# Kernel tuning notes

Hardware: AMD Instinct MI355X
Metric: run time of the kernel (lower is better)

Reference implementation:

```python
import jax, jax.numpy as jnp
import numpy as np

NEG_SLOPE = 0.2
BN_EPS = 1e-5


def gat_conv(x, W_src, W_dst, att_src, att_dst, bias, src, dst, num_nodes):
    # PyG GATConv, heads=1, concat=True, self-loops already included in (src,dst)
    h_src = x @ W_src                      # [N, H]
    h_dst = x @ W_dst                      # [N, H]
    a_src = h_src @ att_src                # [N]
    a_dst = h_dst @ att_dst                # [N]
    e = jax.nn.leaky_relu(a_src[src] + a_dst[dst], NEG_SLOPE)   # [E]
    # segment softmax over incoming edges of each dst node
    m = jax.ops.segment_max(e, dst, num_segments=num_nodes)     # [N]
    p = jnp.exp(e - m[dst])
    denom = jax.ops.segment_sum(p, dst, num_segments=num_nodes) # [N]
    alpha = p / denom[dst]                                      # [E]
    msgs = alpha[:, None] * h_src[src]                           # [E, H]
    out = jax.ops.segment_sum(msgs, dst, num_segments=num_nodes)
    return out + bias


def setup_inputs() -> dict:
    key = jax.random.key(0)
    ks = jax.random.split(key, 20)
    N, D_IN, H1, H2, FC, C = 100000, 256, 128, 128, 64, 40
    E = 1600000
    inp = {}
    inp['x'] = jax.random.normal(ks[0], (N, D_IN), dtype=jnp.float32)
    inp['edge_index'] = jax.random.randint(ks[1], (2, E), 0, N, dtype=jnp.int64)
    s = 1.0 / np.sqrt(D_IN)
    inp['W1_src'] = jax.random.uniform(ks[2], (D_IN, H1), jnp.float32, -s, s)
    inp['W1_dst'] = jax.random.uniform(ks[3], (D_IN, H1), jnp.float32, -s, s)
    inp['att1_src'] = jax.random.normal(ks[4], (H1,), jnp.float32) * 0.1
    inp['att1_dst'] = jax.random.normal(ks[5], (H1,), jnp.float32) * 0.1
    inp['b1'] = jnp.zeros((H1,), jnp.float32)
    s = 1.0 / np.sqrt(H1)
    inp['W2_src'] = jax.random.uniform(ks[6], (H1, H2), jnp.float32, -s, s)
    inp['W2_dst'] = jax.random.uniform(ks[7], (H1, H2), jnp.float32, -s, s)
    inp['att2_src'] = jax.random.normal(ks[8], (H2,), jnp.float32) * 0.1
    inp['att2_dst'] = jax.random.normal(ks[9], (H2,), jnp.float32) * 0.1
    inp['b2'] = jnp.zeros((H2,), jnp.float32)
    s = 1.0 / np.sqrt(H2)
    inp['fc1_w'] = jax.random.uniform(ks[10], (H2, FC), jnp.float32, -s, s)
    inp['fc1_b'] = jax.random.uniform(ks[11], (FC,), jnp.float32, -s, s)
    inp['gamma'] = jnp.ones((FC,), jnp.float32)
    inp['beta'] = jnp.zeros((FC,), jnp.float32)
    s = 1.0 / np.sqrt(FC)
    inp['fc2_w'] = jax.random.uniform(ks[12], (FC, C), jnp.float32, -s, s)
    inp['fc2_b'] = jax.random.uniform(ks[13], (C,), jnp.float32, -s, s)
    return inp


def reference(x, edge_index, W1_src, W1_dst, att1_src, att1_dst, b1,
              W2_src, W2_dst, att2_src, att2_dst, b2,
              fc1_w, fc1_b, gamma, beta, fc2_w, fc2_b):
    N = x.shape[0]
    loops = jnp.arange(N, dtype=edge_index.dtype)
    src = jnp.concatenate([edge_index[0], loops])
    dst = jnp.concatenate([edge_index[1], loops])
    h = jax.nn.relu(gat_conv(x, W1_src, W1_dst, att1_src, att1_dst, b1, src, dst, N))
    h = jax.nn.relu(gat_conv(h, W2_src, W2_dst, att2_src, att2_dst, b2, src, dst, N))
    h = h @ fc1_w + fc1_b                   # [N, 64]
    mu = jnp.mean(h, axis=0)
    var = jnp.var(h, axis=0)
    h = (h - mu) * jax.lax.rsqrt(var + BN_EPS) * gamma + beta
    h = jax.nn.relu(h)
    h = h @ fc2_w + fc2_b                   # [N, C]
    return jax.nn.log_softmax(h, axis=-1)
```

## Files before the change

### kernel.cpp

```cpp
#include <hip/hip_runtime.h>
#include <cstddef>

#define LSLOPE 0.2f
#define BN_EPS 1e-5f

__device__ __forceinline__ float lrelu(float x) { return x > 0.f ? x : LSLOPE * x; }

using half4 = __attribute__((ext_vector_type(4))) _Float16;
using half8 = __attribute__((ext_vector_type(8))) _Float16;
using f32x4 = __attribute__((ext_vector_type(4))) float;

struct h2 { _Float16 h, l; };
__device__ __forceinline__ h2 split2h(float x) {
  h2 r;
  r.h = (_Float16)x;
  r.l = (_Float16)(x - (float)r.h);
  return r;
}

__device__ __forceinline__ unsigned short f2bf(float x) {
  unsigned u = __float_as_uint(x);
  unsigned r = (u + 0x7fffu + ((u >> 16) & 1u)) >> 16;
  return (unsigned short)r;
}
__device__ __forceinline__ float bflo(unsigned int u) { return __uint_as_float(u << 16); }
__device__ __forceinline__ float bfhi(unsigned int u) { return __uint_as_float(u & 0xffff0000u); }

__device__ __forceinline__ void bfrag_body(const float* __restrict__ B, _Float16* __restrict__ bh,
                                           _Float16* __restrict__ bl, int K, int M, int t) {
  int KB = K >> 5;
  int CTF = M >> 4;
  int lane = t & 63;
  int ckb  = t >> 6;
  int c  = ckb / KB, kb = ckb % KB;
  int mr = lane & 15, quad = lane >> 4;
  int col = c * 16 + mr;
  size_t obase = ((size_t)kb * CTF + c) * 512 + (size_t)lane * 8;
#pragma unroll
  for (int j = 0; j < 8; ++j) {
    int k = kb * 32 + quad * 8 + j;
    h2 s = split2h(B[(size_t)k * M + col]);
    bh[obase + j] = s.h;
    bl[obase + j] = s.l;
  }
}

__device__ __forceinline__ void matvec_body(const float* __restrict__ A, const float* __restrict__ v,
                                            float* __restrict__ out, int R, int K, int t) {
  int w = t >> 6;
  int lane = t & 63;
  if (w >= R) return;
  const float* row = A + (size_t)w * K;
  float s = 0.f;
  for (int k = lane; k < K; k += 64) s = fmaf(row[k], v[k], s);
#pragma unroll
  for (int off = 32; off; off >>= 1) s += __shfl_xor(s, off, 64);
  if (lane == 0) out[w] = s;
}

__global__ __launch_bounds__(256) void prep_k(const float* __restrict__ W1s, const float* __restrict__ W2s,
                                              const float* __restrict__ fc1w,
                                              const float* __restrict__ W1d, const float* __restrict__ att1d,
                                              const float* __restrict__ W2d, const float* __restrict__ att2d,
                                              const float* __restrict__ att1s, const float* __restrict__ att2s,
                                              _Float16* B1h, _Float16* B1l, _Float16* B2h, _Float16* B2l,
                                              _Float16* Bfh, _Float16* Bfl,
                                              float* wvd1, float* wvd2, float* wvs1, float* wvs2) {
  int b = blockIdx.x;
  int tid = threadIdx.x;
  if (b < 16)       bfrag_body(W1s, B1h, B1l, 256, 128, b * 256 + tid);
  else if (b < 24)  bfrag_body(W2s, B2h, B2l, 128, 128, (b - 16) * 256 + tid);
  else if (b < 28)  bfrag_body(fc1w, Bfh, Bfl, 128, 64, (b - 24) * 256 + tid);
  else if (b < 92)  matvec_body(W1d, att1d, wvd1, 256, 128, (b - 28) * 256 + tid);
  else if (b < 124) matvec_body(W2d, att2d, wvd2, 128, 128, (b - 92) * 256 + tid);
  else if (b < 188) matvec_body(W1s, att1s, wvs1, 256, 128, (b - 124) * 256 + tid);
  else              matvec_body(W2s, att2s, wvs2, 128, 128, (b - 188) * 256 + tid);
}

template<int K, int MCOLS, bool PS>
__global__ __launch_bounds__(256) void gemm_sk(const float* __restrict__ Af,
                                               const _Float16* __restrict__ Ah,
                                               const _Float16* __restrict__ Al,
                                               const _Float16* __restrict__ Bh,
                                               const _Float16* __restrict__ Bl,
                                               float* __restrict__ Cf,
                                               unsigned short* __restrict__ Cbf,
                                               const float* __restrict__ wvs,
                                               float* __restrict__ asrc,
                                               const float* __restrict__ wvd,
                                               float* __restrict__ adout,
                                               int N,
                                               const float* __restrict__ bias) {
  constexpr int KB   = K / 32;
  constexpr int HALF = MCOLS / 2;
  constexpr int CT   = HALF / 16;
  constexpr int CTF  = MCOLS / 16;
  constexpr int BCH  = CTF / 4;
  __shared__ __align__(16) _Float16 sAh[2][64 * 32];
  __shared__ __align__(16) _Float16 sAl[2][64 * 32];
  __shared__ __align__(16) _Float16 sBh[2][CTF * 512];
  __shared__ __align__(16) _Float16 sBl[2][CTF * 512];
  const int tid  = threadIdx.x;
  const int row0 = blockIdx.x * 64;
  const int wv   = tid >> 6;
  const int wm   = wv >> 1;
  const int wn   = wv & 1;
  const int lane = tid & 63;
  const int quad = lane >> 4;
  const int mr   = lane & 15;

  f32x4 acc[2][CT];
#pragma unroll
  for (int r = 0; r < 2; ++r)
#pragma unroll
    for (int c = 0; c < CT; ++c) acc[r][c] = (f32x4){0.f, 0.f, 0.f, 0.f};
  float pas[2] = {0.f, 0.f}, pad[2] = {0.f, 0.f};

  auto stage_b = [&](int buf, int kbs) {
    const size_t gb = (size_t)kbs * (CTF * 512) + (size_t)lane * 8;
#pragma unroll
    for (int pch = 0; pch < BCH; ++pch) {
      const int ch = wv * BCH + pch;
      __builtin_amdgcn_global_load_lds(
          (const __attribute__((address_space(1))) void*)(Bh + gb + (size_t)ch * 512),
          (__attribute__((address_space(3))) void*)&sBh[buf][ch * 512], 16, 0, 0);
      __builtin_amdgcn_global_load_lds(
          (const __attribute__((address_space(1))) void*)(Bl + gb + (size_t)ch * 512),
          (__attribute__((address_space(3))) void*)&sBl[buf][ch * 512], 16, 0, 0);
    }
  };

  int srow, skc, soff;
  bool sok;
  if (PS) {
    srow = tid >> 2;
    skc  = (tid & 3) << 3;
  } else {
    srow = tid >> 3;
    skc  = (tid & 7) << 2;
  }
  soff = srow * 32 + ((skc + srow * 8) & 31);
  sok  = (row0 + srow) < N;
  int srow2 = 0, skc2 = 0, soff2 = 0;
  bool sok2 = false;
  if (!PS) {
    int s = tid + 256;
    srow2 = s >> 3;
    skc2  = (s & 7) << 2;
    soff2 = srow2 * 32 + ((skc2 + srow2 * 8) & 31);
    sok2  = (row0 + srow2) < N;
  }

  const float4 zf4 = make_float4(0.f, 0.f, 0.f, 0.f);
  const uint4  zu4 = make_uint4(0u, 0u, 0u, 0u);

  stage_b(0, 0);

  {
    if (PS) {
      size_t go = (size_t)(row0 + srow) * K + skc;
      uint4 h0 = sok ? *(const uint4*)&Ah[go] : zu4;
      uint4 l0 = sok ? *(const uint4*)&Al[go] : zu4;
      *(uint4*)&sAh[0][soff] = h0;
      *(uint4*)&sAl[0][soff] = l0;
    } else {
      float4 f0 = sok  ? *(const float4*)&Af[(size_t)(row0 + srow) * K + skc]   : zf4;
      float4 f1 = sok2 ? *(const float4*)&Af[(size_t)(row0 + srow2) * K + skc2] : zf4;
      h2 s0 = split2h(f0.x), s1 = split2h(f0.y), s2 = split2h(f0.z), s3 = split2h(f0.w);
      half4 h4, l4;
      h4[0] = s0.h; h4[1] = s1.h; h4[2] = s2.h; h4[3] = s3.h;
      l4[0] = s0.l; l4[1] = s1.l; l4[2] = s2.l; l4[3] = s3.l;
      *(half4*)&sAh[0][soff] = h4;
      *(half4*)&sAl[0][soff] = l4;
      h2 t0 = split2h(f1.x), t1 = split2h(f1.y), t2 = split2h(f1.z), t3 = split2h(f1.w);
      h4[0] = t0.h; h4[1] = t1.h; h4[2] = t2.h; h4[3] = t3.h;
      l4[0] = t0.l; l4[1] = t1.l; l4[2] = t2.l; l4[3] = t3.l;
      *(half4*)&sAh[0][soff2] = h4;
      *(half4*)&sAl[0][soff2] = l4;
    }
  }

  float4 fa0 = zf4, fa1 = zf4, fb0 = zf4, fb1 = zf4;
  uint4  uah = zu4, ual = zu4, ubh = zu4, ubl = zu4;
  if (KB > 1) {
    const int kn = 32;
    if (PS) {
      size_t go = (size_t)(row0 + srow) * K + kn + skc;
      uah = sok ? *(const uint4*)&Ah[go] : zu4;
      ual = sok ? *(const uint4*)&Al[go] : zu4;
    } else {
      fa0 = sok  ? *(const float4*)&Af[(size_t)(row0 + srow) * K + kn + skc]   : zf4;
      fa1 = sok2 ? *(const float4*)&Af[(size_t)(row0 + srow2) * K + kn + skc2] : zf4;
    }
  }
  __syncthreads();

  const size_t cstride = (size_t)KB * 512;

  for (int kb = 0; kb < KB; ++kb) {
    const int cur = kb & 1, nxt = cur ^ 1;
    const int kk = kb << 5;
    if (kb + 1 < KB) stage_b(nxt, kb + 1);
    if (kb + 2 < KB) {
      const int kn = (kb + 2) << 5;
      if (PS) {
        size_t go = (size_t)(row0 + srow) * K + kn + skc;
        ubh = sok ? *(const uint4*)&Ah[go] : zu4;
        ubl = sok ? *(const uint4*)&Al[go] : zu4;
      } else {
        fb0 = sok  ? *(const float4*)&Af[(size_t)(row0 + srow) * K + kn + skc]   : zf4;
        fb1 = sok2 ? *(const float4*)&Af[(size_t)(row0 + srow2) * K + kn + skc2] : zf4;
      }
    }

    half8 ah[2], al[2];
#pragma unroll
    for (int r = 0; r < 2; ++r) {
      int row = wm * 32 + r * 16 + mr;
      int off = row * 32 + ((quad + row) & 3) * 8;
      ah[r] = *(const half8*)&sAh[cur][off];
      al[r] = *(const half8*)&sAl[cur][off];
    }
    if (wn == 0 && (wvs || wvd)) {
#pragma unroll
      for (int j = 0; j < 8; ++j) {
        const float vs = wvs ? wvs[kk + quad * 8 + j] : 0.f;
        const float vd = wvd ? wvd[kk + quad * 8 + j] : 0.f;
#pragma unroll
        for (int r = 0; r < 2; ++r) {
          const float av = (float)ah[r][j] + (float)al[r][j];
          if (wvs) pas[r] = fmaf(av, vs, pas[r]);
          if (wvd) pad[r] = fmaf(av, vd, pad[r]);
        }
      }
    }
#pragma unroll
    for (int c = 0; c < CT; ++c) {
      const half8 bh = *(const half8*)&sBh[cur][(wn * CT + c) * 512 + lane * 8];
      const half8 bl = *(const half8*)&sBl[cur][(wn * CT + c) * 512 + lane * 8];
#pragma unroll
      for (int r = 0; r < 2; ++r) {
        f32x4 a = acc[r][c];
        a = __builtin_amdgcn_mfma_f32_16x16x32_f16(al[r], bh, a, 0, 0, 0);
        a = __builtin_amdgcn_mfma_f32_16x16x32_f16(ah[r], bl, a, 0, 0, 0);
        a = __builtin_amdgcn_mfma_f32_16x16x32_f16(ah[r], bh, a, 0, 0, 0);
        acc[r][c] = a;
      }
    }
    if (kb + 1 < KB) {
      if (PS) {
        *(uint4*)&sAh[nxt][soff] = uah;
        *(uint4*)&sAl[nxt][soff] = ual;
        uah = ubh; ual = ubl;
      } else {
        h2 s0 = split2h(fa0.x), s1 = split2h(fa0.y), s2 = split2h(fa0.z), s3 = split2h(fa0.w);
        half4 h4, l4;
        h4[0] = s0.h; h4[1] = s1.h; h4[2] = s2.h; h4[3] = s3.h;
        l4[0] = s0.l; l4[1] = s1.l; l4[2] = s2.l; l4[3] = s3.l;
        *(half4*)&sAh[nxt][soff] = h4;
        *(half4*)&sAl[nxt][soff] = l4;
        h2 t0 = split2h(fa1.x), t1 = split2h(fa1.y), t2 = split2h(fa1.z), t3 = split2h(fa1.w);
        h4[0] = t0.h; h4[1] = t1.h; h4[2] = t2.h; h4[3] = t3.h;
        l4[0] = t0.l; l4[1] = t1.l; l4[2] = t2.l; l4[3] = t3.l;
        *(half4*)&sAh[nxt][soff2] = h4;
        *(half4*)&sAl[nxt][soff2] = l4;
        fa0 = fb0; fa1 = fb1;
      }
    }
    __syncthreads();
  }

#pragma unroll
  for (int r = 0; r < 2; ++r)
#pragma unroll
    for (int c = 0; c < CT; ++c) {
      const int gcol = wn * HALF + c * 16 + mr;
      const float bv = bias ? bias[gcol] : 0.f;
#pragma unroll
      for (int q = 0; q < 4; ++q) {
        const int grow = row0 + wm * 32 + r * 16 + quad * 4 + q;
        if (grow < N) {
          float val = acc[r][c][q] + bv;
          if (Cf)  Cf[(size_t)grow * MCOLS + gcol] = val;
          if (Cbf) Cbf[(size_t)grow * 128 + gcol] = f2bf(val);
        }
      }
    }
  if (wn == 0 && wvs) {
#pragma unroll
    for (int r = 0; r < 2; ++r) {
      float d = pas[r];
      d += __shfl_xor(d, 16, 64);
      d += __shfl_xor(d, 32, 64);
      const int grow = row0 + wm * 32 + r * 16 + mr;
      if (quad == 0 && grow < N) asrc[grow] = d;
    }
  }
  if (wn == 0 && wvd) {
#pragma unroll
    for (int r = 0; r < 2; ++r) {
      float d = pad[r];
      d += __shfl_xor(d, 16, 64);
      d += __shfl_xor(d, 32, 64);
      const int grow = row0 + wm * 32 + r * 16 + mr;
      if (quad == 0 && grow < N) adout[grow] = d;
    }
  }
}

__global__ void deg_count_k(const int* __restrict__ edst, int E, int N, int* __restrict__ deg) {
  int i = blockIdx.x * 256 + threadIdx.x;
  if (i >= E + N) return;
  int d = (i < E) ? edst[i] : (i - E);
  atomicAdd(&deg[d], 1);
}

__global__ __launch_bounds__(1024) void scan1_k(const int* __restrict__ deg, int n,
                                                int* __restrict__ ex, int* __restrict__ bsum) {
  __shared__ int sm[1024];
  int t = threadIdx.x;
  int idx = blockIdx.x * 1024 + t;
  int v = (idx < n) ? deg[idx] : 0;
  sm[t] = v;
  __syncthreads();
  for (int off = 1; off < 1024; off <<= 1) {
    int tv = (t >= off) ? sm[t - off] : 0;
    __syncthreads();
    sm[t] += tv;
    __syncthreads();
  }
  if (idx < n) ex[idx] = sm[t] - v;
  if (t == 1023) bsum[blockIdx.x] = sm[t];
}

__global__ void scan3_k(int* __restrict__ ex, const int* __restrict__ bsum, int n, int nb, int total,
                        int* __restrict__ cursor) {
  __shared__ int pbase[2];
  int idx = blockIdx.x * 256 + threadIdx.x;
  int bin0 = (blockIdx.x * 256) >> 10;
  if (threadIdx.x < 2) {
    int b = bin0 + threadIdx.x;
    int s = 0;
    for (int i = 0; i < b && i < nb; ++i) s += bsum[i];
    pbase[threadIdx.x] = s;
  }
  __syncthreads();
  if (idx < n) {
    int v = ex[idx] + pbase[(idx >> 10) - bin0];
    ex[idx] = v;
    cursor[idx] = v;
  }
  if (idx == 0) ex[n] = total;
}

__global__ void scatter_range_k(const int* __restrict__ esrc, const int* __restrict__ edst,
                                int E, int N, int d0, int d1,
                                int* __restrict__ cursor, int* __restrict__ csr_src) {
  int i = blockIdx.x * 256 + threadIdx.x;
  if (i >= E + N) return;
  int d = (i < E) ? edst[i] : (i - E);
  if (d < d0 || d >= d1) return;
  int s = (i < E) ? esrc[i] : d;
  int pos = atomicAdd(&cursor[d], 1);
  csr_src[pos] = s;
}

__global__ __launch_bounds__(256) void gat_agg_k(const unsigned short* __restrict__ hbf,
                                                 const float* __restrict__ a_src,
                                                 const float* __restrict__ a_dst, const int* __restrict__ rowstart,
                                                 const int* __restrict__ csr_src, const float* __restrict__ bias,
                                                 _Float16* __restrict__ oh, _Float16* __restrict__ ol,
                                                 const float* __restrict__ wvd, float* __restrict__ ad_out,
                                                 int N) {
  int w = (blockIdx.x * blockDim.x + threadIdx.x) >> 6;
  int lane = threadIdx.x & 63;
  if (w >= N) return;
  int s0 = rowstart[w];
  int s1 = rowstart[w + 1];
  int deg = s1 - s0;
  float ad = a_dst[w];

  int sA = 0;
  float eA = -3.0e38f;
  if (lane < deg) {
    sA = csr_src[s0 + lane];
    eA = lrelu(a_src[sA] + ad);
  }
  float m = eA;
  for (int j = s0 + 64 + lane; j < s1; j += 64) {
    int s = csr_src[j];
    m = fmaxf(m, lrelu(a_src[s] + ad));
  }
#pragma unroll
  for (int off = 32; off; off >>= 1) m = fmaxf(m, __shfl_xor(m, off, 64));

  float preg = (lane < deg) ? __expf(eA - m) : 0.f;
  float den = preg;
  for (int j = s0 + 64 + lane; j < s1; j += 64) {
    int s = csr_src[j];
    den += __expf(lrelu(a_src[s] + ad) - m);
  }
#pragma unroll
  for (int off = 32; off; off >>= 1) den += __shfl_xor(den, off, 64);
  float inv = 1.f / den;

  const int q  = lane >> 4;
  const int sl = lane & 15;
  const uint4* hrow4 = (const uint4*)hbf;
  float acc[8];
#pragma unroll
  for (int i = 0; i < 8; ++i) acc[i] = 0.f;

  int lim  = deg < 64 ? deg : 64;
  int lim4 = (lim + 3) & ~3;
  int   sP = __shfl(sA, q, 64);
  float wP = __shfl(preg, q, 64) * inv;
  uint4 uP = hrow4[(size_t)sP * 16 + sl];
  for (int jj = 4; jj < lim4; jj += 4) {
    int   sN = __shfl(sA, jj + q, 64);
    float wN = __shfl(preg, jj + q, 64) * inv;
    uint4 uN = hrow4[(size_t)sN * 16 + sl];
    acc[0] = fmaf(wP, bflo(uP.x), acc[0]);
    acc[1] = fmaf(wP, bfhi(uP.x), acc[1]);
    acc[2] = fmaf(wP, bflo(uP.y), acc[2]);
    acc[3] = fmaf(wP, bfhi(uP.y), acc[3]);
    acc[4] = fmaf(wP, bflo(uP.z), acc[4]);
    acc[5] = fmaf(wP, bfhi(uP.z), acc[5]);
    acc[6] = fmaf(wP, bflo(uP.w), acc[6]);
    acc[7] = fmaf(wP, bfhi(uP.w), acc[7]);
    uP = uN; wP = wN;
  }
  acc[0] = fmaf(wP, bflo(uP.x), acc[0]);
  acc[1] = fmaf(wP, bfhi(uP.x), acc[1]);
  acc[2] = fmaf(wP, bflo(uP.y), acc[2]);
  acc[3] = fmaf(wP, bfhi(uP.y), acc[3]);
  acc[4] = fmaf(wP, bflo(uP.z), acc[4]);
  acc[5] = fmaf(wP, bfhi(uP.z), acc[5]);
  acc[6] = fmaf(wP, bflo(uP.w), acc[6]);
  acc[7] = fmaf(wP, bfhi(uP.w), acc[7]);

  for (int j = s0 + 64 + q; j < s1; j += 4) {
    int s = csr_src[j];
    float wgt = __expf(lrelu(a_src[s] + ad) - m) * inv;
    uint4 u = hrow4[(size_t)s * 16 + sl];
    acc[0] = fmaf(wgt, bflo(u.x), acc[0]);
    acc[1] = fmaf(wgt, bfhi(u.x), acc[1]);
    acc[2] = fmaf(wgt, bflo(u.y), acc[2]);
    acc[3] = fmaf(wgt, bfhi(u.y), acc[3]);
    acc[4] = fmaf(wgt, bflo(u.z), acc[4]);
    acc[5] = fmaf(wgt, bfhi(u.z), acc[5]);
    acc[6] = fmaf(wgt, bflo(u.w), acc[6]);
    acc[7] = fmaf(wgt, bfhi(u.w), acc[7]);
  }
#pragma unroll
  for (int i = 0; i < 8; ++i) {
    acc[i] += __shfl_xor(acc[i], 16, 64);
    acc[i] += __shfl_xor(acc[i], 32, 64);
  }
  if (q == 0) {
    float4 b0 = *(const float4*)&bias[8 * sl];
    float4 b1 = *(const float4*)&bias[8 * sl + 4];
    float v[8];
    v[0] = fmaxf(acc[0] + b0.x, 0.f);
    v[1] = fmaxf(acc[1] + b0.y, 0.f);
    v[2] = fmaxf(acc[2] + b0.z, 0.f);
    v[3] = fmaxf(acc[3] + b0.w, 0.f);
    v[4] = fmaxf(acc[4] + b1.x, 0.f);
    v[5] = fmaxf(acc[5] + b1.y, 0.f);
    v[6] = fmaxf(acc[6] + b1.z, 0.f);
    v[7] = fmaxf(acc[7] + b1.w, 0.f);
    half8 vh, vl;
#pragma unroll
    for (int i = 0; i < 8; ++i) {
      h2 s = split2h(v[i]);
      vh[i] = s.h;
      vl[i] = s.l;
    }
    size_t base = (size_t)w * 128 + 8 * sl;
    *(half8*)&oh[base] = vh;
    *(half8*)&ol[base] = vl;
    if (wvd) {
      float4 w0 = *(const float4*)&wvd[8 * sl];
      float4 w1 = *(const float4*)&wvd[8 * sl + 4];
      float dd = v[0] * w0.x + v[1] * w0.y + v[2] * w0.z + v[3] * w0.w
               + v[4] * w1.x + v[5] * w1.y + v[6] * w1.z + v[7] * w1.w;
      dd += __shfl_xor(dd, 1, 64);
      dd += __shfl_xor(dd, 2, 64);
      dd += __shfl_xor(dd, 4, 64);
      dd += __shfl_xor(dd, 8, 64);
      if (sl == 0) ad_out[w] = dd;
    }
  }
}

__global__ __launch_bounds__(256) void bn_stats_k(const float* __restrict__ z, int N,
                                                  float* __restrict__ sums, float* __restrict__ sumsq) {
  __shared__ float ls[256], lq[256];
  int col = threadIdx.x & 63;
  int rg = threadIdx.x >> 6;
  float s = 0.f, q = 0.f;
  for (int r = blockIdx.x * 4 + rg; r < N; r += gridDim.x * 4) {
    float v = z[(size_t)r * 64 + col];
    s += v;
    q = fmaf(v, v, q);
  }
  ls[threadIdx.x] = s;
  lq[threadIdx.x] = q;
  __syncthreads();
  if (threadIdx.x < 64) {
    s = ls[col] + ls[col + 64] + ls[col + 128] + ls[col + 192];
    q = lq[col] + lq[col + 64] + lq[col + 128] + lq[col + 192];
    atomicAdd(&sums[col], s);
    atomicAdd(&sumsq[col], q);
  }
}

__global__ __launch_bounds__(256) void fc2_lsm_k(const float* __restrict__ z,
                                                 const float* __restrict__ sums, const float* __restrict__ sumsq,
                                                 const float* __restrict__ gamma, const float* __restrict__ beta,
                                                 const float* __restrict__ w,
                                                 const float* __restrict__ b, float* __restrict__ out,
                                                 int N, float invN) {
  __shared__ float ssc[64], ssh[64];
  if (threadIdx.x < 64) {
    int c = threadIdx.x;
    float mean = sums[c] * invN;
    float var = sumsq[c] * invN - mean * mean;
    float rs = rsqrtf(var + BN_EPS);
    float sc = gamma[c] * rs;
    ssc[c] = sc;
    ssh[c] = beta[c] - mean * sc;
  }
  __syncthreads();
  int n = blockIdx.x * 256 + threadIdx.x;
  if (n >= N) return;
  float o[40];
#pragma unroll
  for (int c = 0; c < 40; ++c) o[c] = b[c];
  const float* zr = z + (size_t)n * 64;
  for (int k = 0; k < 64; ++k) {
    float v = fmaxf(fmaf(zr[k], ssc[k], ssh[k]), 0.f);
#pragma unroll
    for (int c = 0; c < 40; ++c) o[c] = fmaf(v, w[k * 40 + c], o[c]);
  }
  float mx = o[0];
#pragma unroll
  for (int c = 1; c < 40; ++c) mx = fmaxf(mx, o[c]);
  float s = 0.f;
#pragma unroll
  for (int c = 0; c < 40; ++c) s += __expf(o[c] - mx);
  float ls = __logf(s);
  float* orow = out + (size_t)n * 40;
#pragma unroll
  for (int c = 0; c < 40; ++c) orow[c] = o[c] - mx - ls;
}

static inline char* al16(char* p) { return (char*)(((size_t)p + 15) & ~(size_t)15); }

extern "C" void kernel_launch(void* const* d_in, const int* in_sizes, int n_in,
                              void* d_out, int out_size, void* d_ws, size_t ws_size,
                              hipStream_t stream) {
  const float* x     = (const float*)d_in[0];
  const int*   eidx  = (const int*)d_in[1];
  const float* W1s   = (const float*)d_in[2];
  const float* W1d   = (const float*)d_in[3];
  const float* att1s = (const float*)d_in[4];
  const float* att1d = (const float*)d_in[5];
  const float* b1    = (const float*)d_in[6];
  const float* W2s   = (const float*)d_in[7];
  const float* W2d   = (const float*)d_in[8];
  const float* att2s = (const float*)d_in[9];
  const float* att2d = (const float*)d_in[10];
  const float* b2    = (const float*)d_in[11];
  const float* fc1w  = (const float*)d_in[12];
  const float* fc1b  = (const float*)d_in[13];
  const float* gamma = (const float*)d_in[14];
  const float* beta  = (const float*)d_in[15];
  const float* fc2w  = (const float*)d_in[16];
  const float* fc2b  = (const float*)d_in[17];
  float* out = (float*)d_out;

  const int N  = in_sizes[0] / 256;
  const int E  = in_sizes[1] / 2;
  const int ET = E + N;

  char* p = (char*)d_ws;
  int* deg      = (int*)p;     p += (size_t)N * 4;
  float* sums   = (float*)p;   p += 64 * 4;
  float* sumsq  = (float*)p;   p += 64 * 4;
  unsigned short* bhA = (unsigned short*)p; p += (size_t)N * 128 * 2;
  _Float16* hAh = (_Float16*)p;  p += (size_t)N * 128 * 2;
  _Float16* hAl = (_Float16*)p;  p += (size_t)N * 128 * 2;
  float* hF = (float*)p;         p += (size_t)N * 64 * 4;
  int* rowstart = (int*)p;     p += (size_t)(N + 1) * 4;
  int* cursor   = (int*)p;     p += (size_t)N * 4;
  int* csr_src  = (int*)p;     p += (size_t)ET * 4;
  float* a_src  = (float*)p;   p += (size_t)N * 4;
  float* a_dst  = (float*)p;   p += (size_t)N * 4;
  float* a_dst2 = (float*)p;   p += (size_t)N * 4;
  float* wvd1   = (float*)p;   p += 256 * 4;
  float* wvd2   = (float*)p;   p += 128 * 4;
  float* wvs1   = (float*)p;   p += 256 * 4;
  float* wvs2   = (float*)p;   p += 128 * 4;
  int* bsum     = (int*)p;     p += 256 * 4;
  p = al16(p);
  _Float16* B1h = (_Float16*)p; p += (size_t)256 * 128 * 2;
  _Float16* B1l = (_Float16*)p; p += (size_t)256 * 128 * 2;
  _Float16* B2h = (_Float16*)p; p += (size_t)128 * 128 * 2;
  _Float16* B2l = (_Float16*)p; p += (size_t)128 * 128 * 2;
  _Float16* Bfh = (_Float16*)p; p += (size_t)128 * 64 * 2;
  _Float16* Bfl = (_Float16*)p; p += (size_t)128 * 64 * 2;

  const int* esrc = eidx;
  const int* edst = eidx + E;

  hipMemsetAsync(deg, 0, (size_t)N * 4 + 512, stream);

  deg_count_k<<<(ET + 255) / 256, 256, 0, stream>>>(edst, E, N, deg);
  int nb = (N + 1023) / 1024;
  scan1_k<<<nb, 1024, 0, stream>>>(deg, N, rowstart, bsum);
  scan3_k<<<(N + 255) / 256, 256, 0, stream>>>(rowstart, bsum, N, nb, ET, cursor);
  {
    const int NR = 8;
    int step = (N + NR - 1) / NR;
    for (int r = 0; r < NR; ++r) {
      int d0 = r * step;
      int d1 = d0 + step < N ? d0 + step : N;
      scatter_range_k<<<(ET + 255) / 256, 256, 0, stream>>>(esrc, edst, E, N, d0, d1, cursor, csr_src);
    }
  }

  prep_k<<<220, 256, 0, stream>>>(W1s, W2s, fc1w, W1d, att1d, W2d, att2d, att1s, att2s,
                                  B1h, B1l, B2h, B2l, Bfh, Bfl, wvd1, wvd2, wvs1, wvs2);

  const int gdk = (N + 63) / 64;

  gemm_sk<256, 128, false><<<gdk, 256, 0, stream>>>(x, nullptr, nullptr, B1h, B1l,
                                                    nullptr, bhA, wvs1, a_src, wvd1, a_dst, N, nullptr);
  gat_agg_k<<<(N + 3) / 4, 256, 0, stream>>>(bhA, a_src, a_dst, rowstart, csr_src, b1,
                                             hAh, hAl, wvd2, a_dst2, N);

  gemm_sk<128, 128, true><<<gdk, 256, 0, stream>>>(nullptr, hAh, hAl, B2h, B2l,
                                                   nullptr, bhA, wvs2, a_src, nullptr, nullptr, N, nullptr);
  gat_agg_k<<<(N + 3) / 4, 256, 0, stream>>>(bhA, a_src, a_dst2, rowstart, csr_src, b2,
                                             hAh, hAl, nullptr, nullptr, N);

  gemm_sk<128, 64, true><<<gdk, 256, 0, stream>>>(nullptr, hAh, hAl, Bfh, Bfl,
                                                  hF, nullptr, nullptr, nullptr, nullptr, nullptr, N, fc1b);
  bn_stats_k<<<512, 256, 0, stream>>>(hF, N, sums, sumsq);
  fc2_lsm_k<<<(N + 255) / 256, 256, 0, stream>>>(hF, sums, sumsq, gamma, beta, fc2w, fc2b, out,
                                                 N, 1.0f / (float)N);
}
```

Before: 678.0 us.

## Fuse fc1 linear layer into second GAT aggregation epilogue

The second gat_agg_k call now stages each node's 128-wide ReLU output in shared memory and computes the 64-wide fc1 projection in fp32 FMA per wave, writing hF directly. This removes the separate fc1 GEMM launch, the split-fp16 hAh/hAl write and reread, and the fc1 weight fragment preparation. In exchange, each wave performs a scalar 128x64 dot loop that reads fc1w from global or L2 memory rather than using matrix cores. Early-returning waves and the lgkmcnt wait without a block barrier are correct only because each wave reads just its own slab row.

```diff
diff --git a/kernel.cpp b/kernel.cpp
--- a/kernel.cpp
+++ b/kernel.cpp
@@ -59,22 +59,19 @@
 }
 
 __global__ __launch_bounds__(256) void prep_k(const float* __restrict__ W1s, const float* __restrict__ W2s,
-                                              const float* __restrict__ fc1w,
                                               const float* __restrict__ W1d, const float* __restrict__ att1d,
                                               const float* __restrict__ W2d, const float* __restrict__ att2d,
                                               const float* __restrict__ att1s, const float* __restrict__ att2s,
                                               _Float16* B1h, _Float16* B1l, _Float16* B2h, _Float16* B2l,
-                                              _Float16* Bfh, _Float16* Bfl,
                                               float* wvd1, float* wvd2, float* wvs1, float* wvs2) {
   int b = blockIdx.x;
   int tid = threadIdx.x;
   if (b < 16)       bfrag_body(W1s, B1h, B1l, 256, 128, b * 256 + tid);
   else if (b < 24)  bfrag_body(W2s, B2h, B2l, 128, 128, (b - 16) * 256 + tid);
-  else if (b < 28)  bfrag_body(fc1w, Bfh, Bfl, 128, 64, (b - 24) * 256 + tid);
-  else if (b < 92)  matvec_body(W1d, att1d, wvd1, 256, 128, (b - 28) * 256 + tid);
-  else if (b < 124) matvec_body(W2d, att2d, wvd2, 128, 128, (b - 92) * 256 + tid);
-  else if (b < 188) matvec_body(W1s, att1s, wvs1, 256, 128, (b - 124) * 256 + tid);
-  else              matvec_body(W2s, att2s, wvs2, 128, 128, (b - 188) * 256 + tid);
+  else if (b < 88)  matvec_body(W1d, att1d, wvd1, 256, 128, (b - 24) * 256 + tid);
+  else if (b < 120) matvec_body(W2d, att2d, wvd2, 128, 128, (b - 88) * 256 + tid);
+  else if (b < 184) matvec_body(W1s, att1s, wvs1, 256, 128, (b - 120) * 256 + tid);
+  else              matvec_body(W2s, att2s, wvs2, 128, 128, (b - 184) * 256 + tid);
 }
 
 template<int K, int MCOLS, bool PS>
@@ -195,8 +192,6 @@
   }
   __syncthreads();
 
-  const size_t cstride = (size_t)KB * 512;
-
   for (int kb = 0; kb < KB; ++kb) {
     const int cur = kb & 1, nxt = cur ^ 1;
     const int kk = kb << 5;
@@ -371,9 +366,14 @@
                                                  const int* __restrict__ csr_src, const float* __restrict__ bias,
                                                  _Float16* __restrict__ oh, _Float16* __restrict__ ol,
                                                  const float* __restrict__ wvd, float* __restrict__ ad_out,
-                                                 int N) {
+                                                 int N,
+                                                 const float* __restrict__ fc1w,
+                                                 const float* __restrict__ fc1b,
+                                                 float* __restrict__ hF) {
+  __shared__ float slab[4][128];
   int w = (blockIdx.x * blockDim.x + threadIdx.x) >> 6;
   int lane = threadIdx.x & 63;
+  int wvz = threadIdx.x >> 6;
   if (w >= N) return;
   int s0 = rowstart[w];
   int s1 = rowstart[w + 1];
@@ -469,27 +469,42 @@
     v[5] = fmaxf(acc[5] + b1.y, 0.f);
     v[6] = fmaxf(acc[6] + b1.z, 0.f);
     v[7] = fmaxf(acc[7] + b1.w, 0.f);
-    half8 vh, vl;
-#pragma unroll
-    for (int i = 0; i < 8; ++i) {
-      h2 s = split2h(v[i]);
-      vh[i] = s.h;
-      vl[i] = s.l;
-    }
-    size_t base = (size_t)w * 128 + 8 * sl;
-    *(half8*)&oh[base] = vh;
-    *(half8*)&ol[base] = vl;
-    if (wvd) {
-      float4 w0 = *(const float4*)&wvd[8 * sl];
-      float4 w1 = *(const float4*)&wvd[8 * sl + 4];
-      float dd = v[0] * w0.x + v[1] * w0.y + v[2] * w0.z + v[3] * w0.w
-               + v[4] * w1.x + v[5] * w1.y + v[6] * w1.z + v[7] * w1.w;
-      dd += __shfl_xor(dd, 1, 64);
-      dd += __shfl_xor(dd, 2, 64);
-      dd += __shfl_xor(dd, 4, 64);
-      dd += __shfl_xor(dd, 8, 64);
-      if (sl == 0) ad_out[w] = dd;
-    }
+    if (fc1w) {
+#pragma unroll
+      for (int i = 0; i < 8; ++i) slab[wvz][8 * sl + i] = v[i];
+    } else {
+      half8 vh, vl;
+#pragma unroll
+      for (int i = 0; i < 8; ++i) {
+        h2 s = split2h(v[i]);
+        vh[i] = s.h;
+        vl[i] = s.l;
+      }
+      size_t base = (size_t)w * 128 + 8 * sl;
+      *(half8*)&oh[base] = vh;
+      *(half8*)&ol[base] = vl;
+      if (wvd) {
+        float4 w0 = *(const float4*)&wvd[8 * sl];
+        float4 w1 = *(const float4*)&wvd[8 * sl + 4];
+        float dd = v[0] * w0.x + v[1] * w0.y + v[2] * w0.z + v[3] * w0.w
+                 + v[4] * w1.x + v[5] * w1.y + v[6] * w1.z + v[7] * w1.w;
+        dd += __shfl_xor(dd, 1, 64);
+        dd += __shfl_xor(dd, 2, 64);
+        dd += __shfl_xor(dd, 4, 64);
+        dd += __shfl_xor(dd, 8, 64);
+        if (sl == 0) ad_out[w] = dd;
+      }
+    }
+  }
+  if (fc1w) {
+    asm volatile("s_waitcnt lgkmcnt(0)" ::: "memory");
+    __builtin_amdgcn_sched_barrier(0);
+    float o = fc1b[lane];
+    const float* wcol = fc1w + lane;
+#pragma unroll 8
+    for (int k = 0; k < 128; ++k)
+      o = fmaf(slab[wvz][k], wcol[(size_t)k * 64], o);
+    hF[(size_t)w * 64 + lane] = o;
   }
 }
 
@@ -608,8 +623,6 @@
   _Float16* B1l = (_Float16*)p; p += (size_t)256 * 128 * 2;
   _Float16* B2h = (_Float16*)p; p += (size_t)128 * 128 * 2;
   _Float16* B2l = (_Float16*)p; p += (size_t)128 * 128 * 2;
-  _Float16* Bfh = (_Float16*)p; p += (size_t)128 * 64 * 2;
-  _Float16* Bfl = (_Float16*)p; p += (size_t)128 * 64 * 2;
 
   const int* esrc = eidx;
   const int* edst = eidx + E;
@@ -630,23 +643,23 @@
     }
   }
 
-  prep_k<<<220, 256, 0, stream>>>(W1s, W2s, fc1w, W1d, att1d, W2d, att2d, att1s, att2s,
-                                  B1h, B1l, B2h, B2l, Bfh, Bfl, wvd1, wvd2, wvs1, wvs2);
+  prep_k<<<216, 256, 0, stream>>>(W1s, W2s, W1d, att1d, W2d, att2d, att1s, att2s,
+                                  B1h, B1l, B2h, B2l, wvd1, wvd2, wvs1, wvs2);
 
   const int gdk = (N + 63) / 64;
 
   gemm_sk<256, 128, false><<<gdk, 256, 0, stream>>>(x, nullptr, nullptr, B1h, B1l,
                                                     nullptr, bhA, wvs1, a_src, wvd1, a_dst, N, nullptr);
   gat_agg_k<<<(N + 3) / 4, 256, 0, stream>>>(bhA, a_src, a_dst, rowstart, csr_src, b1,
-                                             hAh, hAl, wvd2, a_dst2, N);
+                                             hAh, hAl, wvd2, a_dst2, N,
+                                             nullptr, nullptr, nullptr);
 
   gemm_sk<128, 128, true><<<gdk, 256, 0, stream>>>(nullptr, hAh, hAl, B2h, B2l,
                                                    nullptr, bhA, wvs2, a_src, nullptr, nullptr, N, nullptr);
   gat_agg_k<<<(N + 3) / 4, 256, 0, stream>>>(bhA, a_src, a_dst2, rowstart, csr_src, b2,
-                                             hAh, hAl, nullptr, nullptr, N);
-
-  gemm_sk<128, 64, true><<<gdk, 256, 0, stream>>>(nullptr, hAh, hAl, Bfh, Bfl,
-                                                  hF, nullptr, nullptr, nullptr, nullptr, nullptr, N, fc1b);
+                                             nullptr, nullptr, nullptr, nullptr, N,
+                                             fc1w, fc1b, hF);
+
   bn_stats_k<<<512, 256, 0, stream>>>(hF, N, sums, sumsq);
   fc2_lsm_k<<<(N + 255) / 256, 256, 0, stream>>>(hF, sums, sumsq, gamma, beta, fc2w, fc2b, out,
                                                  N, 1.0f / (float)N);
```

Result: slower. 725.0 us (+6.9%).
